# Kernel optimization log

Measured on AMD Instinct MI355X. Metric: run time of the kernel, lower is better.

Reference implementation:

```python
import jax, jax.numpy as jnp
import numpy as np

SCALE = 4          # cfg['stride']
S = 7              # rcnn_crop_size
MAX_SIDE = 64      # max proposal side length in voxels (matches setup_inputs)
# max feature-space crop length = MAX_SIDE/SCALE + 2 (floor/ceil expansion) = 18
WMAX = int(np.ceil((MAX_SIDE // SCALE + 2) / S)) + 1  # = 4, adaptive-pool window bound


def setup_inputs() -> dict:
    key = jax.random.key(0)
    k1, k2, k3, k4 = jax.random.split(key, 4)
    B, C = 2, 128
    D, H, W = 128, 256, 256
    f = jax.random.normal(k1, (B, C, D // SCALE, H // SCALE, W // SCALE), jnp.float32)
    inputs = jnp.zeros((B, 1, D, H, W), jnp.float32)  # only shape is used by forward
    N = 32
    b = jax.random.randint(k2, (N,), 0, B).astype(jnp.float32)
    score = jnp.ones((N,), jnp.float32)
    cz = jax.random.uniform(k3, (N,), minval=32.0, maxval=float(D - 32))
    cy = jax.random.uniform(jax.random.fold_in(k3, 1), (N,), minval=32.0, maxval=float(H - 32))
    cx = jax.random.uniform(jax.random.fold_in(k3, 2), (N,), minval=32.0, maxval=float(W - 32))
    sides = jax.random.randint(k4, (N, 3), 16, MAX_SIDE + 1).astype(jnp.float32)
    proposals = jnp.stack([b, score, cz, cy, cx, sides[:, 0], sides[:, 1], sides[:, 2]], axis=1)
    return {"f": f, "inputs": inputs, "proposals": proposals}


def _crop_pool(f, b, c0, L, feat_dims):
    """Adaptive max-pool3d of f[b, :, c0:c0+L] to [C,S,S,S] via fixed-size masked windows."""
    i = jnp.arange(S)
    # torch adaptive pooling: start=floor(i*L/S), end=ceil((i+1)*L/S)
    start = (i[:, None] * L[None, :]) // S                       # [S,3]
    end = ((i[:, None] + 1) * L[None, :] + S - 1) // S           # [S,3]
    idx = c0[None, :, None] + start[:, :, None] + jnp.arange(WMAX)[None, None, :]  # [S,3,WMAX]
    valid = idx < (c0[None, :, None] + end[:, :, None])
    idx = jnp.minimum(idx, jnp.asarray(feat_dims, jnp.int32)[None, :, None] - 1)
    iz, iy, ix = idx[:, 0], idx[:, 1], idx[:, 2]                 # each [S,WMAX]
    vz, vy, vx = valid[:, 0], valid[:, 1], valid[:, 2]
    # gather [C, S, WMAX, S, WMAX, S, WMAX]
    g = f[b][:, iz[:, :, None, None, None, None],
             iy[None, None, :, :, None, None],
             ix[None, None, None, None, :, :]]
    m = (vz[:, :, None, None, None, None]
         & vy[None, None, :, :, None, None]
         & vx[None, None, None, None, :, :])
    g = jnp.where(m[None], g, -jnp.inf)
    return g.max(axis=(2, 4, 6))  # [C, S, S, S]


def reference(f, inputs, proposals):
    D, H, W = inputs.shape[2:]
    feat_dims = (D // SCALE, H // SCALE, W // SCALE)
    b = proposals[:, 0].astype(jnp.int32)
    center = proposals[:, 2:5]
    side = proposals[:, 5:8]
    c0 = jnp.floor((center - side / 2) / SCALE).astype(jnp.int32)
    c1 = jnp.ceil((center + side / 2) / SCALE).astype(jnp.int32)
    lim = jnp.asarray(feat_dims, jnp.int32)
    c0 = jnp.maximum(c0, 0)
    c1 = jnp.minimum(c1, lim[None, :])
    L = c1 - c0  # [N,3] crop lengths per axis
    pooled = jax.vmap(lambda bb, cc, ll: _crop_pool(f, bb, cc, ll, feat_dims))(b, c0, L)
    return pooled  # [N, C, S, S, S]
```

## Files before the change

kernel.cpp:

```cpp
#include <hip/hip_runtime.h>
#include <math.h>


constexpr int C_CH = 128;
constexpr int FD = 32, FH = 64, FW = 64;
constexpr int CH_VOL = FD * FH * FW;
constexpr int LMAX = 17;
constexpr int XPAD = 20;
constexpr int VQ   = XPAD / 4;
constexpr int PLQ  = LMAX * VQ;
constexpr int THREADS = 384;

__global__ __launch_bounds__(THREADS) void crop_roi_kernel(
    const float* __restrict__ f,
    const float* __restrict__ proposals,
    float* __restrict__ out)
{
    __shared__ __align__(16) float lds[LMAX * LMAX * XPAD];
    __shared__ int ws_[3][7], we_[3][7];

    const int n = blockIdx.x;
    const int c = blockIdx.y;

    const float* p = proposals + n * 8;
    const int   b  = (int)p[0];
    const float cz = p[2], cy = p[3], cx = p[4];
    const float sz = p[5], sy = p[6], sx = p[7];

    const int c0z = max((int)floorf((cz - sz * 0.5f) * 0.25f), 0);
    const int c0y = max((int)floorf((cy - sy * 0.5f) * 0.25f), 0);
    const int c0x = max((int)floorf((cx - sx * 0.5f) * 0.25f), 0);
    const int c1z = min((int)ceilf((cz + sz * 0.5f) * 0.25f), FD);
    const int c1y = min((int)ceilf((cy + sy * 0.5f) * 0.25f), FH);
    const int c1x = min((int)ceilf((cx + sx * 0.5f) * 0.25f), FW);
    const int Lz = c1z - c0z, Ly = c1y - c0y, Lx = c1x - c0x;

    if (threadIdx.x < 21) {
        const int d = threadIdx.x / 7;
        const int i = threadIdx.x % 7;
        const int L = (d == 0) ? Lz : (d == 1) ? Ly : Lx;
        ws_[d][i] = (i * L) / 7;
        we_[d][i] = ((i + 1) * L + 6) / 7;
    }

    const int ax0   = c0x & ~3;
    const int shift = c0x - ax0;
    const int nvec  = (shift + Lx + 3) >> 2;

    const float4* f4 = reinterpret_cast<const float4*>(
        f + (size_t)(b * C_CH + c) * CH_VOL + c0z * (FH * FW) + c0y * FW + ax0);
    float4* lds4 = reinterpret_cast<float4*>(lds);

    const int tot = Lz * PLQ;
    for (int v = threadIdx.x; v < tot; v += THREADS) {
        const int z = v / PLQ;
        const int r = v - z * PLQ;
        const int y = r / VQ;
        const int q = r - y * VQ;
        if (y < Ly && q < nvec) {
            lds4[v] = f4[z * (FH * FW / 4) + y * (FW / 4) + q];
        }
    }
    __syncthreads();

    const int r = threadIdx.x;
    if (r < 343) {
        const int iz = r / 49, iy = (r / 7) % 7, ix = r % 7;
        const int zs = ws_[0][iz], ze = we_[0][iz];
        const int ys = ws_[1][iy], ye = we_[1][iy];
        const int xs = ws_[2][ix] + shift, xm = we_[2][ix] - 1 + shift;
        const int x1 = min(xs + 1, xm);
        const int x2 = min(xs + 2, xm);
        const int x3 = min(xs + 3, xm);

        float m = -INFINITY;
        for (int z = zs; z < ze; ++z) {
            for (int y = ys; y < ye; ++y) {
                const float* Lp = lds + (z * LMAX + y) * XPAD;
                const float t = fmaxf(fmaxf(Lp[xs], Lp[x1]), Lp[x2]);
                m = fmaxf(fmaxf(t, Lp[x3]), m);
            }
        }
        out[(size_t)(n * C_CH + c) * 343 + r] = m;
    }
}

extern "C" void kernel_launch(void* const* d_in, const int* in_sizes, int n_in,
                              void* d_out, int out_size, void* d_ws, size_t ws_size,
                              hipStream_t stream) {
    const float* f         = (const float*)d_in[0];
    const float* proposals = (const float*)d_in[2];
    float* out             = (float*)d_out;

    dim3 grid(32, C_CH);
    crop_roi_kernel<<<grid, THREADS, 0, stream>>>(f, proposals, out);
}
```

Measured before the change: 210.9 us.

## Stage crop tile into LDS with direct global_load_lds and compact layout

Replaces the register-staged float4 copy loop with the AMD global_load_lds builtin, so 16-byte chunks go straight from global memory into LDS without passing through VGPRs. The LDS tile is packed densely by the actual Ly instead of the padded LMAX row count. Index decoding uses a multiply-shift reciprocal in place of divisions, and out-of-range lanes are clamped rather than predicated, because the builtin needs uniform per-wave participation. This adds redundant clamped loads and relies on the 16-byte direct-to-LDS variant being supported on this hardware.

```diff
diff --git a/kernel.cpp b/kernel.cpp
--- a/kernel.cpp
+++ b/kernel.cpp
@@ -8,15 +8,21 @@
 constexpr int LMAX = 17;
 constexpr int XPAD = 20;
 constexpr int VQ   = XPAD / 4;
-constexpr int PLQ  = LMAX * VQ;
 constexpr int THREADS = 384;
+constexpr int MAXQ = ((LMAX * LMAX * VQ + THREADS - 1) / THREADS) * THREADS;
+
+__device__ __forceinline__ void gload_lds16(const void* g, void* l) {
+    __builtin_amdgcn_global_load_lds(
+        (const __attribute__((address_space(1))) unsigned int*)g,
+        (__attribute__((address_space(3))) unsigned int*)l, 16, 0, 0);
+}
 
 __global__ __launch_bounds__(THREADS) void crop_roi_kernel(
     const float* __restrict__ f,
     const float* __restrict__ proposals,
     float* __restrict__ out)
 {
-    __shared__ __align__(16) float lds[LMAX * LMAX * XPAD];
+    __shared__ __align__(16) float lds[MAXQ * 4];
     __shared__ int ws_[3][7], we_[3][7];
 
     const int n = blockIdx.x;
@@ -43,23 +49,26 @@
         we_[d][i] = ((i + 1) * L + 6) / 7;
     }
 
-    const int ax0   = c0x & ~3;
-    const int shift = c0x - ax0;
-    const int nvec  = (shift + Lx + 3) >> 2;
+    const int ax0    = c0x & ~3;
+    const int shift  = c0x - ax0;
+    const int nvecm1 = ((shift + Lx + 3) >> 2) - 1;
 
     const float4* f4 = reinterpret_cast<const float4*>(
         f + (size_t)(b * C_CH + c) * CH_VOL + c0z * (FH * FW) + c0y * FW + ax0);
     float4* lds4 = reinterpret_cast<float4*>(lds);
 
-    const int tot = Lz * PLQ;
-    for (int v = threadIdx.x; v < tot; v += THREADS) {
-        const int z = v / PLQ;
-        const int r = v - z * PLQ;
-        const int y = r / VQ;
-        const int q = r - y * VQ;
-        if (y < Ly && q < nvec) {
-            lds4[v] = f4[z * (FH * FW / 4) + y * (FW / 4) + q];
-        }
+    const unsigned Mly = 16777216u / (unsigned)Ly + 1u;
+    const int tot = Lz * Ly * VQ;
+
+    for (int base = 0; base < tot; base += THREADS) {
+        const unsigned v  = (unsigned)min(base + (int)threadIdx.x, tot - 1);
+        const unsigned zy = v / 5u;
+        const int q  = (int)(v - zy * 5u);
+        const int z  = (int)((zy * Mly) >> 24);
+        const int y  = (int)zy - z * Ly;
+        const int qc = min(q, nvecm1);
+        gload_lds16(f4 + (z * (FH * FW / 4) + y * (FW / 4) + qc),
+                    lds4 + (base + (int)threadIdx.x));
     }
     __syncthreads();
 
@@ -75,8 +84,9 @@
 
         float m = -INFINITY;
         for (int z = zs; z < ze; ++z) {
+            const float* Pz = lds + (z * Ly) * XPAD;
             for (int y = ys; y < ye; ++y) {
-                const float* Lp = lds + (z * LMAX + y) * XPAD;
+                const float* Lp = Pz + y * XPAD;
                 const float t = fmaxf(fmaxf(Lp[xs], Lp[x1]), Lp[x2]);
                 m = fmaxf(fmaxf(t, Lp[x3]), m);
             }
```

Result: faster. 205.6 us (-2.5%).
